# Kernel optimization log

Measured on AMD Instinct MI355X. Metric: run time of the kernel, lower is better.

## Reference

```python
import jax, jax.numpy as jnp
import numpy as np
from jax import lax

COMMITMENT_COST = 0.25

def setup_inputs() -> dict:
    key = jax.random.key(0)
    k1, k2, k3, k4 = jax.random.split(key, 4)
    B, C, H, W, K = 32, 128, 32, 32, 8192
    return {
        "x": jax.random.normal(k1, (B, C, H, W), dtype=jnp.float32),
        "W_lin": jax.random.normal(k2, (C, C), dtype=jnp.float32) * (1.0 / np.sqrt(C)),
        "b_lin": jax.random.normal(k3, (C,), dtype=jnp.float32) * 0.01,
        "emb": jax.random.normal(k4, (K, C), dtype=jnp.float32),
    }

def reference(x, W_lin, b_lin, emb):
    B, C, H, W = x.shape
    K = emb.shape[0]
    # BCHW -> BHWC, then linear projection
    inp = jnp.transpose(x, (0, 2, 3, 1))          # [B,H,W,C]
    inp = inp @ W_lin.T + b_lin                   # nn.Linear
    flat = inp.reshape(-1, C)                     # [N,C], N=B*H*W
    # squared L2 distances to codebook: ||z||^2 + ||e||^2 - 2 z.e
    d = (jnp.sum(flat**2, axis=1, keepdims=True)
         + jnp.sum(emb**2, axis=1)
         - 2.0 * flat @ emb.T)                    # [N,K]
    idx = jnp.argmin(d, axis=1)                   # [N]
    quantized = emb[idx].reshape(inp.shape)       # gather == onehot @ emb
    e_latent = jnp.mean((lax.stop_gradient(quantized) - inp) ** 2)
    q_latent = jnp.mean((quantized - lax.stop_gradient(inp)) ** 2)
    loss = q_latent + COMMITMENT_COST * e_latent
    # straight-through estimator
    quantized_st = inp + lax.stop_gradient(quantized - inp)
    # perplexity from code usage histogram (== mean of one-hot encodings)
    counts = jnp.zeros((K,), dtype=flat.dtype).at[idx].add(1.0)
    avg_probs = counts / flat.shape[0]
    perplexity = jnp.exp(-jnp.sum(avg_probs * jnp.log(avg_probs + 1e-10)))
    out = jnp.transpose(quantized_st, (0, 3, 1, 2))  # back to BCHW
    return (loss, out, perplexity, idx[:, None])
```

## Files before the change

kernel.cpp:

```cpp
#include <hip/hip_runtime.h>
#include <hip/hip_bf16.h>
#include <float.h>

#define NPIX   32768
#define CDIM   128
#define KCB    8192
#define EPS_STOP 0.30f
#define TAUF   0.012f
#define RCAP   8192
#define RCAPA  2048

typedef _Float16 f16x8 __attribute__((ext_vector_type(8)));
typedef float    f32x16 __attribute__((ext_vector_type(16)));

#define WS_EMBFH   0
#define WS_E2      2359296
#define WS_ZWS     2392064
#define WS_CAND    19169280
#define WS_IDX     20217856
#define WS_RLISTA  20348928
#define WS_RLISTB  20381696
#define WS_SCAND   20512768
#define WS_SCANI   21037056
#define WS_COUNTS  21299200
#define WS_LOSS    21331968
#define WS_RCNTA   21331972
#define WS_RCNTB   21331976
#define WS_ZERO_OFF 21299200
#define WS_ZERO_LEN 32780

#define OUT_OFF_OUT  1
#define OUT_OFF_PERP 4194305
#define OUT_OFF_IDX  4194306

__device__ __forceinline__ float min3f(float a, float b, float c) {
    return fminf(fminf(a, b), c);
}

__device__ __forceinline__ void ins6(float f, float v[6]) {
    float a = fmaxf(v[0], f); v[0] = fminf(v[0], f);
    float b = fmaxf(v[1], a); v[1] = fminf(v[1], a);
    a = fmaxf(v[2], b); v[2] = fminf(v[2], b);
    b = fmaxf(v[3], a); v[3] = fminf(v[3], a);
    a = fmaxf(v[4], b); v[4] = fminf(v[4], b);
    v[5] = fminf(v[5], a);
}

__device__ __forceinline__ float packmin(float m, uint32_t id) {
    return __uint_as_float((__float_as_uint(m) & 0xFFFFFE00u) | id);
}

__global__ __launch_bounds__(256) void k_prep2(const float* __restrict__ emb,
                                               _Float16* __restrict__ embFh,
                                               int* __restrict__ zerobuf) {
    const int t = threadIdx.x, w = t >> 6, l = t & 63;
    if (blockIdx.x < 9) {
        int idx0 = blockIdx.x * 1024 + t * 4;
        #pragma unroll
        for (int k = 0; k < 4; ++k)
            if (idx0 + k < 8195) zerobuf[idx0 + k] = 0;
    }
    __shared__ float rs[4][128];
    const int m = blockIdx.x * 4 + w;
    const float2 v = *(const float2*)&emb[(size_t)m * 128 + l * 2];
    rs[w][l * 2] = v.x; rs[w][l * 2 + 1] = v.y;
    float s = v.x * v.x + v.y * v.y;
    #pragma unroll
    for (int o = 32; o; o >>= 1) s += __shfl_down(s, o, 64);
    const float e2v = __shfl(s, 0, 64);

    f16x8 hv;
    #pragma unroll
    for (int j = 0; j < 8; ++j) hv[j] = (_Float16)0.0f;
    if (l < 16) {
        const float* rp = &rs[w][l * 8];
        #pragma unroll
        for (int j = 0; j < 8; ++j) hv[j] = (_Float16)(-2.0f * rp[j]);
    } else if (l == 16) {
        float vv = e2v + 512.0f;
        _Float16 eh = (_Float16)vv;
        hv[0] = eh;
        hv[1] = (_Float16)(vv - (float)eh);
    }
    if (l < 18) {
        const int s_ = l >> 1, h_ = l & 1;
        size_t base = (((size_t)(m >> 5) * 9 + s_) * 64 + (m & 31) + h_ * 32) * 8;
        *(f16x8*)&embFh[base] = hv;
    }
}

__global__ __launch_bounds__(256, 2) void k_main(
    const float* __restrict__ x, const float* __restrict__ Wl, const float* __restrict__ bl,
    const _Float16* __restrict__ embFh,
    float* __restrict__ zws, float4* __restrict__ cand)
{
    __shared__ __align__(16) float As[64 * 132];
    __shared__ __align__(16) float Xs[64 * 66];
    __shared__ float z2p[256];

    const int t  = threadIdx.x;
    const int n0 = blockIdx.x * 64;
    const int b  = n0 >> 10;
    const int hw0 = n0 & 1023;

    {
        const int p = t & 63, ig = t >> 6;
        float accz[32];
        const float4* bl4 = (const float4*)(bl + ig * 32);
        #pragma unroll
        for (int q = 0; q < 8; ++q) {
            float4 v = bl4[q];
            accz[4*q+0] = v.x; accz[4*q+1] = v.y; accz[4*q+2] = v.z; accz[4*q+3] = v.w;
        }
        for (int hf = 0; hf < 2; ++hf) {
            __syncthreads();
            for (int r = 0; r < 16; ++r) {
                int lin = r * 256 + t;
                int cc = lin >> 6, pp = lin & 63;
                Xs[cc * 66 + pp] = x[(size_t)(b * 128 + hf * 64 + cc) * 1024 + hw0 + pp];
            }
            __syncthreads();
            for (int cc4 = 0; cc4 < 16; ++cc4) {
                float xv0 = Xs[(cc4*4+0) * 66 + p];
                float xv1 = Xs[(cc4*4+1) * 66 + p];
                float xv2 = Xs[(cc4*4+2) * 66 + p];
                float xv3 = Xs[(cc4*4+3) * 66 + p];
                #pragma unroll
                for (int ii = 0; ii < 32; ++ii) {
                    const float4 w4 = *(const float4*)&Wl[(size_t)(ig*32+ii) * 128 + hf*64 + cc4*4];
                    float a = accz[ii];
                    a = fmaf(w4.x, xv0, a);
                    a = fmaf(w4.y, xv1, a);
                    a = fmaf(w4.z, xv2, a);
                    a = fmaf(w4.w, xv3, a);
                    accz[ii] = a;
                }
            }
        }
        float ssq = 0.f;
        float4* ao = (float4*)&As[p * 132 + ig * 32];
        float4* zo = (float4*)(zws + (size_t)(n0 + p) * 128 + ig * 32);
        #pragma unroll
        for (int q = 0; q < 8; ++q) {
            float4 v = make_float4(accz[4*q+0], accz[4*q+1], accz[4*q+2], accz[4*q+3]);
            ao[q] = v;
            zo[q] = v;
            ssq = fmaf(v.x, v.x, fmaf(v.y, v.y, fmaf(v.z, v.z, fmaf(v.w, v.w, ssq))));
        }
        z2p[p * 4 + ig] = ssq;
    }
    __syncthreads();

    const int l = t & 63, w = t >> 6;
    const int half = l >> 5, pcol = l & 31;
    f16x8 B0[9], B1[9];
    #pragma unroll
    for (int nt = 0; nt < 2; ++nt) {
        int p = nt * 32 + pcol;
        #pragma unroll
        for (int s = 0; s < 8; ++s) {
            const float* zp = &As[p * 132 + s * 16 + half * 8];
            float4 v0 = *(const float4*)zp;
            float4 v1 = *(const float4*)(zp + 4);
            float vals[8] = {v0.x, v0.y, v0.z, v0.w, v1.x, v1.y, v1.z, v1.w};
            f16x8 hh;
            #pragma unroll
            for (int j2 = 0; j2 < 8; ++j2) hh[j2] = (_Float16)vals[j2];
            if (nt == 0) B0[s] = hh; else B1[s] = hh;
        }
    }
    {
        f16x8 b8;
        #pragma unroll
        for (int j2 = 0; j2 < 8; ++j2) b8[j2] = (_Float16)0.0f;
        if (half == 0) { b8[0] = (_Float16)1.0f; b8[1] = (_Float16)1.0f; }
        B0[8] = b8; B1[8] = b8;
    }

    auto tree16 = [](const f32x16& v) -> float {
        float a = min3f(v[0], v[1], v[2]);
        float bb = min3f(v[3], v[4], v[5]);
        float c = min3f(v[6], v[7], v[8]);
        float d = min3f(v[9], v[10], v[11]);
        float e = min3f(v[12], v[13], v[14]);
        float f = min3f(a, bb, c);
        float g = min3f(d, e, v[15]);
        return fminf(f, g);
    };

    float gv[6] = {3e38f, 3e38f, 3e38f, 3e38f, 3e38f, 3e38f};
    float hv[6] = {3e38f, 3e38f, 3e38f, 3e38f, 3e38f, 3e38f};
    const f16x8* Ahp = (const f16x8*)embFh;
    f16x8 aE[9], aO[9];
    {
        const f16x8* P = Ahp + (size_t)w * 576 + l;
        #pragma unroll
        for (int s = 0; s < 9; ++s) aE[s] = P[s * 64];
    }
    {
        const f16x8* P = Ahp + (size_t)(w + 4) * 576 + l;
        #pragma unroll
        for (int s = 0; s < 9; ++s) aO[s] = P[s * 64];
    }

    f32x16 e0, e1, o0, o1;
    uint32_t idv = (uint32_t)((w << 1) | half);

    e0 = {}; e1 = {};
    #pragma unroll
    for (int s = 0; s < 9; ++s) {
        e0 = __builtin_amdgcn_mfma_f32_32x32x16_f16(aE[s], B0[s], e0, 0, 0, 0);
        e1 = __builtin_amdgcn_mfma_f32_32x32x16_f16(aE[s], B1[s], e1, 0, 0, 0);
    }

    for (int it = 0; it < 31; ++it) {
        const int g = w + it * 8;
        {
            const f16x8* P = Ahp + (size_t)(g + 8) * 576 + l;
            #pragma unroll
            for (int s = 0; s < 9; ++s) aE[s] = P[s * 64];
        }
        o0 = {}; o1 = {};
        #pragma unroll
        for (int s = 0; s < 9; ++s) {
            o0 = __builtin_amdgcn_mfma_f32_32x32x16_f16(aO[s], B0[s], o0, 0, 0, 0);
            o1 = __builtin_amdgcn_mfma_f32_32x32x16_f16(aO[s], B1[s], o1, 0, 0, 0);
        }
        {
            float m0 = tree16(e0), m1 = tree16(e1);
            ins6(packmin(m0, idv), gv);
            ins6(packmin(m1, idv), hv);
        }
        {
            const f16x8* P = Ahp + (size_t)(g + 12) * 576 + l;
            #pragma unroll
            for (int s = 0; s < 9; ++s) aO[s] = P[s * 64];
        }
        e0 = {}; e1 = {};
        #pragma unroll
        for (int s = 0; s < 9; ++s) {
            e0 = __builtin_amdgcn_mfma_f32_32x32x16_f16(aE[s], B0[s], e0, 0, 0, 0);
            e1 = __builtin_amdgcn_mfma_f32_32x32x16_f16(aE[s], B1[s], e1, 0, 0, 0);
        }
        {
            float m0 = tree16(o0), m1 = tree16(o1);
            ins6(packmin(m0, idv + 8u), gv);
            ins6(packmin(m1, idv + 8u), hv);
        }
        idv += 16u;
    }
    o0 = {}; o1 = {};
    #pragma unroll
    for (int s = 0; s < 9; ++s) {
        o0 = __builtin_amdgcn_mfma_f32_32x32x16_f16(aO[s], B0[s], o0, 0, 0, 0);
        o1 = __builtin_amdgcn_mfma_f32_32x32x16_f16(aO[s], B1[s], o1, 0, 0, 0);
    }
    {
        float m0 = tree16(e0), m1 = tree16(e1);
        ins6(packmin(m0, idv), gv);
        ins6(packmin(m1, idv), hv);
    }
    {
        float m0 = tree16(o0), m1 = tree16(o1);
        ins6(packmin(m0, idv + 8u), gv);
        ins6(packmin(m1, idv + 8u), hv);
    }

    __syncthreads();
    float* Ms = Xs;
    const int slot = (w << 1) | half;
    #pragma unroll
    for (int q = 0; q < 6; ++q) {
        Ms[(pcol * 8 + slot) * 6 + q] = gv[q];
        Ms[((32 + pcol) * 8 + slot) * 6 + q] = hv[q];
    }
    __syncthreads();
    if (t < 64) {
        float v6[6] = {3e38f, 3e38f, 3e38f, 3e38f, 3e38f, 3e38f};
        #pragma unroll
        for (int s = 0; s < 48; ++s) ins6(Ms[t * 48 + s], v6);
        float z2 = z2p[t*4+0] + z2p[t*4+1] + z2p[t*4+2] + z2p[t*4+3];
        cand[(size_t)(n0 + t) * 2 + 0] = make_float4(v6[0], v6[1], v6[2], v6[3]);
        cand[(size_t)(n0 + t) * 2 + 1] = make_float4(v6[4], v6[5], z2, 0.f);
    }
}

__global__ __launch_bounds__(256) void k_rec(
    const float* __restrict__ zws, const float* __restrict__ emb,
    const float4* __restrict__ cand, int* __restrict__ idxws,
    float* __restrict__ out_idxf, float* __restrict__ losssum,
    int* __restrict__ rlistA, int* __restrict__ rcntA,
    int* __restrict__ rlistB, int* __restrict__ rcntB)
{
    __shared__ float lred[16];
    const int t = threadIdx.x;
    const int pl = t >> 4, j = t & 15;
    const int n = blockIdx.x * 16 + pl;

    const float4 za = *(const float4*)&zws[(size_t)n * 128 + j * 8];
    const float4 zb = *(const float4*)&zws[(size_t)n * 128 + j * 8 + 4];
    const float4 c0 = cand[(size_t)n * 2 + 0];
    const float4 c1 = cand[(size_t)n * 2 + 1];
    const float pv[6] = {c0.x, c0.y, c0.z, c0.w, c1.x, c1.y};
    const float pbase = c1.z - 512.0f;

    float d1 = 3e38f, d2 = 3e38f; int i1 = 0x7fffffff, i2 = 0x7fffffff;
    bool safe = false;
    float lastgmin = 0.f;
    for (int q = 0; q < 6; ++q) {
        uint32_t bits = __float_as_uint(pv[q]);
        float gmin = __uint_as_float(bits & 0xFFFFFE00u);
        lastgmin = gmin;
        if (gmin >= d1 - pbase + EPS_STOP) { safe = true; break; }
        const int mbase = (int)((bits >> 1) & 255u) * 32 + (int)((bits & 1u) << 2);
        #pragma unroll
        for (int c = 0; c < 16; ++c) {
            int m = mbase + (c & 3) + 8 * (c >> 2);
            const float4 ea = *(const float4*)&emb[(size_t)m * 128 + j * 8];
            const float4 eb = *(const float4*)&emb[(size_t)m * 128 + j * 8 + 4];
            float da0 = za.x - ea.x, da1 = za.y - ea.y, da2 = za.z - ea.z, da3 = za.w - ea.w;
            float db0 = zb.x - eb.x, db1 = zb.y - eb.y, db2 = zb.z - eb.z, db3 = zb.w - eb.w;
            float s0 = da0*da0; s0 = fmaf(da1, da1, s0); s0 = fmaf(da2, da2, s0); s0 = fmaf(da3, da3, s0);
            float s1 = db0*db0; s1 = fmaf(db1, db1, s1); s1 = fmaf(db2, db2, s1); s1 = fmaf(db3, db3, s1);
            float s = s0 + s1;
            s += __shfl_xor(s, 1, 16);
            s += __shfl_xor(s, 2, 16);
            s += __shfl_xor(s, 4, 16);
            s += __shfl_xor(s, 8, 16);
            if (s < d1 || (s == d1 && m < i1)) { d2 = d1; i2 = i1; d1 = s; i1 = m; }
            else if (s < d2) { d2 = s; i2 = m; }
        }
    }
    if (!safe && lastgmin >= d1 - pbase + EPS_STOP) safe = true;

    if (j == 0) {
        idxws[n] = i1;
        out_idxf[n] = (float)i1;
        if (!safe) {
            int s = atomicAdd(rcntA, 1);
            if (s < RCAPA) rlistA[s] = n;
        } else if ((d2 - d1) < TAUF) {
            int s = atomicAdd(rcntB, 1);
            if (s < RCAP) { int4 v4 = make_int4(n, i1, i2, 0); ((int4*)rlistB)[s] = v4; }
        }
        lred[pl] = d1;
    }
    __syncthreads();
    if (t == 0) {
        float ls = 0.f;
        #pragma unroll
        for (int q = 0; q < 16; ++q) ls += lred[q];
        atomicAdd(losssum, ls);
    }
}

__global__ __launch_bounds__(256) void k_scanp(
    const float* __restrict__ zws, const float* __restrict__ emb,
    const int* __restrict__ rcntA, const int* __restrict__ rlistA,
    double* __restrict__ scand, int* __restrict__ scani)
{
    int cnt = *rcntA; if (cnt > RCAPA) cnt = RCAPA;
    const int t = threadIdx.x;
    const int chunk = blockIdx.x & 31;
    const int gi = t >> 4, j = t & 15;
    __shared__ double sd[16];
    __shared__ int si[16];
    for (int e = blockIdx.x >> 5; e < cnt; e += 64) {
        const int n = rlistA[e];
        const float4 za = *(const float4*)&zws[(size_t)n * 128 + j * 8];
        const float4 zb = *(const float4*)&zws[(size_t)n * 128 + j * 8 + 4];
        double best = 1e300; int bi = 0x7fffffff;
        const int kbase = chunk * 256 + gi * 16;
        for (int c = 0; c < 16; ++c) {
            const int m = kbase + c;
            const float4 ea = *(const float4*)&emb[(size_t)m * 128 + j * 8];
            const float4 eb = *(const float4*)&emb[(size_t)m * 128 + j * 8 + 4];
            double sa = 0.0, sb = 0.0, d;
            d = (double)za.x - (double)ea.x; sa += d * d;
            d = (double)za.y - (double)ea.y; sa += d * d;
            d = (double)za.z - (double)ea.z; sa += d * d;
            d = (double)za.w - (double)ea.w; sa += d * d;
            d = (double)zb.x - (double)eb.x; sb += d * d;
            d = (double)zb.y - (double)eb.y; sb += d * d;
            d = (double)zb.z - (double)eb.z; sb += d * d;
            d = (double)zb.w - (double)eb.w; sb += d * d;
            double s = sa + sb;
            s += __shfl_xor(s, 1, 16);
            s += __shfl_xor(s, 2, 16);
            s += __shfl_xor(s, 4, 16);
            s += __shfl_xor(s, 8, 16);
            if (s < best) { best = s; bi = m; }
        }
        __syncthreads();
        if (j == 0) { sd[gi] = best; si[gi] = bi; }
        __syncthreads();
        if (t == 0) {
            double b = sd[0]; int ib = si[0];
            #pragma unroll
            for (int q = 1; q < 16; ++q)
                if (sd[q] < b || (sd[q] == b && si[q] < ib)) { b = sd[q]; ib = si[q]; }
            scand[e * 32 + chunk] = b;
            scani[e * 32 + chunk] = ib;
        }
    }
}

__global__ __launch_bounds__(128) void k_fix(
    const float* __restrict__ x, const float* __restrict__ Wl, const float* __restrict__ bl,
    const float* __restrict__ emb,
    const int* __restrict__ rcntA, const int* __restrict__ rlistA,
    const double* __restrict__ scand, const int* __restrict__ scani,
    const int* __restrict__ rcntB, const int* __restrict__ rlistB,
    int* __restrict__ idxws, float* __restrict__ out_idxf)
{
    const int t = threadIdx.x;
    if (blockIdx.x < 32) {
        if (t < 64) {
            int cnt = *rcntA; if (cnt > RCAPA) cnt = RCAPA;
            for (int e = blockIdx.x; e < cnt; e += 32) {
                double b = 1e300; int ib = 0x7fffffff;
                if (t < 32) { b = scand[e * 32 + t]; ib = scani[e * 32 + t]; }
                #pragma unroll
                for (int o = 16; o; o >>= 1) {
                    double ob = __shfl_down(b, o, 64);
                    int oi = __shfl_down(ib, o, 64);
                    if (ob < b || (ob == b && oi < ib)) { b = ob; ib = oi; }
                }
                if (t == 0) { int n = rlistA[e]; idxws[n] = ib; out_idxf[n] = (float)ib; }
            }
        }
        return;
    }
    __shared__ double xs[128];
    __shared__ double red[128];
    __shared__ double red2[128];
    int cnt = *rcntB; if (cnt > RCAP) cnt = RCAP;
    for (int e = (int)blockIdx.x - 32; e < cnt; e += 256) {
        const int4 v = ((const int4*)rlistB)[e];
        const int n = v.x, c1 = v.y, c2 = v.z;
        const int b = n >> 10, hw = n & 1023;
        __syncthreads();
        xs[t] = (double)x[(size_t)(b * 128 + t) * 1024 + hw];
        __syncthreads();
        double z0 = (double)bl[t], z1 = 0.0, z2 = 0.0, z3 = 0.0;
        const float* wr = &Wl[(size_t)t * 128];
        #pragma unroll 8
        for (int c = 0; c < 128; c += 4) {
            z0 = fma((double)wr[c + 0], xs[c + 0], z0);
            z1 = fma((double)wr[c + 1], xs[c + 1], z1);
            z2 = fma((double)wr[c + 2], xs[c + 2], z2);
            z3 = fma((double)wr[c + 3], xs[c + 3], z3);
        }
        double z = (z0 + z1) + (z2 + z3);
        double da = z - (double)emb[(size_t)c1 * 128 + t];
        double db = z - (double)emb[(size_t)c2 * 128 + t];
        red[t] = da * da; red2[t] = db * db;
        __syncthreads();
        for (int o = 64; o; o >>= 1) {
            if (t < o) { red[t] += red[t + o]; red2[t] += red2[t + o]; }
            __syncthreads();
        }
        if (t == 0) {
            double d1v = red[0], d2v = red2[0];
            int win = (d2v < d1v || (d2v == d1v && c2 < c1)) ? c2 : c1;
            idxws[n] = win;
            out_idxf[n] = (float)win;
        }
        __syncthreads();
    }
}

__global__ __launch_bounds__(256) void k_out(
    const float* __restrict__ emb, const int* __restrict__ idxws,
    float* __restrict__ outp , float* __restrict__ counts)
{
    const int t = threadIdx.x;
    const int b  = blockIdx.x >> 4;
    const int h2 = blockIdx.x & 15;
    const int pix = t & 63;
    const int cq  = t >> 6;
    const int n = b * 1024 + h2 * 64 + pix;
    const int id = idxws[n];
    if (cq == 0) atomicAdd(&counts[id], 1.0f);
    const float4* ep = (const float4*)&emb[(size_t)id * 128 + cq * 32];
    float* ob = outp + (size_t)b * 131072 + (size_t)cq * 32768 + h2 * 64 + pix;
    #pragma unroll
    for (int c4 = 0; c4 < 8; ++c4) {
        float4 v = ep[c4];
        __builtin_nontemporal_store(v.x, &ob[(c4 * 4 + 0) * 1024]);
        __builtin_nontemporal_store(v.y, &ob[(c4 * 4 + 1) * 1024]);
        __builtin_nontemporal_store(v.z, &ob[(c4 * 4 + 2) * 1024]);
        __builtin_nontemporal_store(v.w, &ob[(c4 * 4 + 3) * 1024]);
    }
}

__global__ __launch_bounds__(256) void k_final(
    const float* __restrict__ counts, const float* __restrict__ losssum, float* __restrict__ d_out)
{
    const int t = threadIdx.x;
    float ent = 0.f;
    for (int k = t; k < KCB; k += 256) {
        float p = counts[k] * (1.0f / 32768.0f);
        ent -= p * logf(p + 1e-10f);
    }
    #pragma unroll
    for (int o = 32; o; o >>= 1) ent += __shfl_down(ent, o, 64);
    __shared__ float wred[4];
    if ((t & 63) == 0) wred[t >> 6] = ent;
    __syncthreads();
    if (t == 0) {
        float e = wred[0] + wred[1] + wred[2] + wred[3];
        d_out[0] = 1.25f * (*losssum) * (1.0f / 4194304.0f);
        d_out[OUT_OFF_PERP] = expf(e);
    }
}

extern "C" void kernel_launch(void* const* d_in, const int* in_sizes, int n_in,
                              void* d_out, int out_size, void* d_ws, size_t ws_size,
                              hipStream_t stream) {
    (void)in_sizes; (void)n_in; (void)out_size; (void)ws_size;
    const float* x   = (const float*)d_in[0];
    const float* Wl  = (const float*)d_in[1];
    const float* bl  = (const float*)d_in[2];
    const float* emb = (const float*)d_in[3];
    float* out = (float*)d_out;
    char*  ws  = (char*)d_ws;

    _Float16* embFh = (_Float16*)(ws + WS_EMBFH);
    float* zws     = (float*)(ws + WS_ZWS);
    float4* cand   = (float4*)(ws + WS_CAND);
    int*   idxws   = (int*)  (ws + WS_IDX);
    int*   rlistA  = (int*)  (ws + WS_RLISTA);
    int*   rlistB  = (int*)  (ws + WS_RLISTB);
    double* scand  = (double*)(ws + WS_SCAND);
    int*   scani   = (int*)  (ws + WS_SCANI);
    float* counts  = (float*)(ws + WS_COUNTS);
    float* losssum = (float*)(ws + WS_LOSS);
    int*   rcntA   = (int*)  (ws + WS_RCNTA);
    int*   rcntB   = (int*)  (ws + WS_RCNTB);
    int*   zerobuf = (int*)  (ws + WS_ZERO_OFF);

    k_prep2<<<KCB / 4, 256, 0, stream>>>(emb, embFh, zerobuf);
    k_main<<<NPIX / 64, 256, 0, stream>>>(x, Wl, bl, embFh, zws, cand);
    k_rec<<<NPIX / 16, 256, 0, stream>>>(zws, emb, cand, idxws, out + OUT_OFF_IDX,
                                         losssum, rlistA, rcntA, rlistB, rcntB);
    k_scanp<<<2048, 256, 0, stream>>>(zws, emb, rcntA, rlistA, scand, scani);
    k_fix<<<288, 128, 0, stream>>>(x, Wl, bl, emb, rcntA, rlistA, scand, scani,
                                   rcntB, rlistB, idxws, out + OUT_OFF_IDX);
    k_out<<<512, 256, 0, stream>>>(emb, idxws, out + OUT_OFF_OUT, counts);
    k_final<<<1, 256, 0, stream>>>(counts, losssum, out);
}
```

Baseline: 275.6 us.

## Fuse candidate rescoring kernel into main distance kernel

Moves the exact fp32 rescoring of the top-6 candidate groups from a separate k_rec kernel into the tail of k_main. Candidates and z are read from shared memory (As, candL) rather than written to and re-read from global memory, and one kernel launch goes away. The cost is extra shared memory per block in a kernel tuned for 2 blocks/CU. The serial 4-pass rescoring loop also lengthens each block's tail, which could lower occupancy or overlap.

```diff
diff --git a/kernel.cpp b/kernel.cpp
--- a/kernel.cpp
+++ b/kernel.cpp
@@ -91,12 +91,16 @@
 
 __global__ __launch_bounds__(256, 2) void k_main(
     const float* __restrict__ x, const float* __restrict__ Wl, const float* __restrict__ bl,
-    const _Float16* __restrict__ embFh,
-    float* __restrict__ zws, float4* __restrict__ cand)
+    const _Float16* __restrict__ embFh, const float* __restrict__ emb,
+    float* __restrict__ zws, int* __restrict__ idxws,
+    float* __restrict__ out_idxf, float* __restrict__ losssum,
+    int* __restrict__ rlistA, int* __restrict__ rcntA,
+    int* __restrict__ rlistB, int* __restrict__ rcntB)
 {
     __shared__ __align__(16) float As[64 * 132];
     __shared__ __align__(16) float Xs[64 * 66];
     __shared__ float z2p[256];
+    __shared__ float candL[64 * 8];
 
     const int t  = threadIdx.x;
     const int n0 = blockIdx.x * 64;
@@ -280,77 +284,75 @@
         #pragma unroll
         for (int s = 0; s < 48; ++s) ins6(Ms[t * 48 + s], v6);
         float z2 = z2p[t*4+0] + z2p[t*4+1] + z2p[t*4+2] + z2p[t*4+3];
-        cand[(size_t)(n0 + t) * 2 + 0] = make_float4(v6[0], v6[1], v6[2], v6[3]);
-        cand[(size_t)(n0 + t) * 2 + 1] = make_float4(v6[4], v6[5], z2, 0.f);
-    }
-}
-
-__global__ __launch_bounds__(256) void k_rec(
-    const float* __restrict__ zws, const float* __restrict__ emb,
-    const float4* __restrict__ cand, int* __restrict__ idxws,
-    float* __restrict__ out_idxf, float* __restrict__ losssum,
-    int* __restrict__ rlistA, int* __restrict__ rcntA,
-    int* __restrict__ rlistB, int* __restrict__ rcntB)
-{
-    __shared__ float lred[16];
-    const int t = threadIdx.x;
-    const int pl = t >> 4, j = t & 15;
-    const int n = blockIdx.x * 16 + pl;
-
-    const float4 za = *(const float4*)&zws[(size_t)n * 128 + j * 8];
-    const float4 zb = *(const float4*)&zws[(size_t)n * 128 + j * 8 + 4];
-    const float4 c0 = cand[(size_t)n * 2 + 0];
-    const float4 c1 = cand[(size_t)n * 2 + 1];
-    const float pv[6] = {c0.x, c0.y, c0.z, c0.w, c1.x, c1.y};
-    const float pbase = c1.z - 512.0f;
-
-    float d1 = 3e38f, d2 = 3e38f; int i1 = 0x7fffffff, i2 = 0x7fffffff;
-    bool safe = false;
-    float lastgmin = 0.f;
-    for (int q = 0; q < 6; ++q) {
-        uint32_t bits = __float_as_uint(pv[q]);
-        float gmin = __uint_as_float(bits & 0xFFFFFE00u);
-        lastgmin = gmin;
-        if (gmin >= d1 - pbase + EPS_STOP) { safe = true; break; }
-        const int mbase = (int)((bits >> 1) & 255u) * 32 + (int)((bits & 1u) << 2);
-        #pragma unroll
-        for (int c = 0; c < 16; ++c) {
-            int m = mbase + (c & 3) + 8 * (c >> 2);
-            const float4 ea = *(const float4*)&emb[(size_t)m * 128 + j * 8];
-            const float4 eb = *(const float4*)&emb[(size_t)m * 128 + j * 8 + 4];
-            float da0 = za.x - ea.x, da1 = za.y - ea.y, da2 = za.z - ea.z, da3 = za.w - ea.w;
-            float db0 = zb.x - eb.x, db1 = zb.y - eb.y, db2 = zb.z - eb.z, db3 = zb.w - eb.w;
-            float s0 = da0*da0; s0 = fmaf(da1, da1, s0); s0 = fmaf(da2, da2, s0); s0 = fmaf(da3, da3, s0);
-            float s1 = db0*db0; s1 = fmaf(db1, db1, s1); s1 = fmaf(db2, db2, s1); s1 = fmaf(db3, db3, s1);
-            float s = s0 + s1;
-            s += __shfl_xor(s, 1, 16);
-            s += __shfl_xor(s, 2, 16);
-            s += __shfl_xor(s, 4, 16);
-            s += __shfl_xor(s, 8, 16);
-            if (s < d1 || (s == d1 && m < i1)) { d2 = d1; i2 = i1; d1 = s; i1 = m; }
-            else if (s < d2) { d2 = s; i2 = m; }
-        }
-    }
-    if (!safe && lastgmin >= d1 - pbase + EPS_STOP) safe = true;
-
-    if (j == 0) {
-        idxws[n] = i1;
-        out_idxf[n] = (float)i1;
-        if (!safe) {
-            int s = atomicAdd(rcntA, 1);
-            if (s < RCAPA) rlistA[s] = n;
-        } else if ((d2 - d1) < TAUF) {
-            int s = atomicAdd(rcntB, 1);
-            if (s < RCAP) { int4 v4 = make_int4(n, i1, i2, 0); ((int4*)rlistB)[s] = v4; }
-        }
-        lred[pl] = d1;
+        #pragma unroll
+        for (int q = 0; q < 6; ++q) candL[t * 8 + q] = v6[q];
+        candL[t * 8 + 6] = z2;
     }
     __syncthreads();
-    if (t == 0) {
-        float ls = 0.f;
-        #pragma unroll
-        for (int q = 0; q < 16; ++q) ls += lred[q];
-        atomicAdd(losssum, ls);
+
+    {
+        const int pl = t >> 4, j = t & 15;
+        float lossacc = 0.f;
+        for (int pass = 0; pass < 4; ++pass) {
+            const int px = pass * 16 + pl;
+            const int n = n0 + px;
+            const float4 za = *(const float4*)&As[px * 132 + j * 8];
+            const float4 zb = *(const float4*)&As[px * 132 + j * 8 + 4];
+            const float* cl = &candL[px * 8];
+            const float pv[6] = {cl[0], cl[1], cl[2], cl[3], cl[4], cl[5]};
+            const float pbase = cl[6] - 512.0f;
+
+            float d1 = 3e38f, d2 = 3e38f; int i1 = 0x7fffffff, i2 = 0x7fffffff;
+            bool safe = false;
+            float lastgmin = 0.f;
+            for (int q = 0; q < 6; ++q) {
+                uint32_t bits = __float_as_uint(pv[q]);
+                float gmin = __uint_as_float(bits & 0xFFFFFE00u);
+                lastgmin = gmin;
+                if (gmin >= d1 - pbase + EPS_STOP) { safe = true; break; }
+                const int mbase = (int)((bits >> 1) & 255u) * 32 + (int)((bits & 1u) << 2);
+                #pragma unroll
+                for (int c = 0; c < 16; ++c) {
+                    int m = mbase + (c & 3) + 8 * (c >> 2);
+                    const float4 ea = *(const float4*)&emb[(size_t)m * 128 + j * 8];
+                    const float4 eb = *(const float4*)&emb[(size_t)m * 128 + j * 8 + 4];
+                    float da0 = za.x - ea.x, da1 = za.y - ea.y, da2 = za.z - ea.z, da3 = za.w - ea.w;
+                    float db0 = zb.x - eb.x, db1 = zb.y - eb.y, db2 = zb.z - eb.z, db3 = zb.w - eb.w;
+                    float s0 = da0*da0; s0 = fmaf(da1, da1, s0); s0 = fmaf(da2, da2, s0); s0 = fmaf(da3, da3, s0);
+                    float s1 = db0*db0; s1 = fmaf(db1, db1, s1); s1 = fmaf(db2, db2, s1); s1 = fmaf(db3, db3, s1);
+                    float s = s0 + s1;
+                    s += __shfl_xor(s, 1, 16);
+                    s += __shfl_xor(s, 2, 16);
+                    s += __shfl_xor(s, 4, 16);
+                    s += __shfl_xor(s, 8, 16);
+                    if (s < d1 || (s == d1 && m < i1)) { d2 = d1; i2 = i1; d1 = s; i1 = m; }
+                    else if (s < d2) { d2 = s; i2 = m; }
+                }
+            }
+            if (!safe && lastgmin >= d1 - pbase + EPS_STOP) safe = true;
+
+            if (j == 0) {
+                idxws[n] = i1;
+                out_idxf[n] = (float)i1;
+                if (!safe) {
+                    int s = atomicAdd(rcntA, 1);
+                    if (s < RCAPA) rlistA[s] = n;
+                } else if ((d2 - d1) < TAUF) {
+                    int s = atomicAdd(rcntB, 1);
+                    if (s < RCAP) { int4 v4 = make_int4(n, i1, i2, 0); ((int4*)rlistB)[s] = v4; }
+                }
+                lossacc += d1;
+            }
+        }
+        __syncthreads();
+        if (j == 0) z2p[pl] = lossacc;
+        __syncthreads();
+        if (t == 0) {
+            float ls = 0.f;
+            #pragma unroll
+            for (int q = 0; q < 16; ++q) ls += z2p[q];
+            atomicAdd(losssum, ls);
+        }
     }
 }
 
@@ -528,7 +530,6 @@
 
     _Float16* embFh = (_Float16*)(ws + WS_EMBFH);
     float* zws     = (float*)(ws + WS_ZWS);
-    float4* cand   = (float4*)(ws + WS_CAND);
     int*   idxws   = (int*)  (ws + WS_IDX);
     int*   rlistA  = (int*)  (ws + WS_RLISTA);
     int*   rlistB  = (int*)  (ws + WS_RLISTB);
@@ -541,9 +542,9 @@
     int*   zerobuf = (int*)  (ws + WS_ZERO_OFF);
 
     k_prep2<<<KCB / 4, 256, 0, stream>>>(emb, embFh, zerobuf);
-    k_main<<<NPIX / 64, 256, 0, stream>>>(x, Wl, bl, embFh, zws, cand);
-    k_rec<<<NPIX / 16, 256, 0, stream>>>(zws, emb, cand, idxws, out + OUT_OFF_IDX,
-                                         losssum, rlistA, rcntA, rlistB, rcntB);
+    k_main<<<NPIX / 64, 256, 0, stream>>>(x, Wl, bl, embFh, emb, zws, idxws,
+                                          out + OUT_OFF_IDX, losssum,
+                                          rlistA, rcntA, rlistB, rcntB);
     k_scanp<<<2048, 256, 0, stream>>>(zws, emb, rcntA, rlistA, scand, scani);
     k_fix<<<288, 128, 0, stream>>>(x, Wl, bl, emb, rcntA, rlistA, scand, scani,
                                    rcntB, rlistB, idxws, out + OUT_OFF_IDX);
```

Measured after the change: 283.9 us. 3.0% more time.

## Split k_main work across 512 threads with one pixel tile per wave

Applied to the files above, without the earlier changes.

Doubles the block size of k_main to 512 threads. Each wave now handles one 32-pixel column tile against a quarter of the codebook, instead of two pixel tiles against an eighth, so each wave keeps a single B fragment set and one top-6 list. The projection is split so each thread computes 16 output channels rather than 32. The goal is to cut register pressure and raise occupancy to hide MFMA and load latency. The cost is that each wave now loads codebook A fragments for half as many MFMAs, doubling codebook global/L2 traffic per block.

```diff
diff --git a/kernel.cpp b/kernel.cpp
--- a/kernel.cpp
+++ b/kernel.cpp
@@ -89,14 +89,14 @@
     }
 }
 
-__global__ __launch_bounds__(256, 2) void k_main(
+__global__ __launch_bounds__(512, 4) void k_main(
     const float* __restrict__ x, const float* __restrict__ Wl, const float* __restrict__ bl,
     const _Float16* __restrict__ embFh,
     float* __restrict__ zws, float4* __restrict__ cand)
 {
     __shared__ __align__(16) float As[64 * 132];
     __shared__ __align__(16) float Xs[64 * 66];
-    __shared__ float z2p[256];
+    __shared__ float z2p[64 * 8];
 
     const int t  = threadIdx.x;
     const int n0 = blockIdx.x * 64;
@@ -105,17 +105,17 @@
 
     {
         const int p = t & 63, ig = t >> 6;
-        float accz[32];
-        const float4* bl4 = (const float4*)(bl + ig * 32);
-        #pragma unroll
-        for (int q = 0; q < 8; ++q) {
+        float accz[16];
+        const float4* bl4 = (const float4*)(bl + ig * 16);
+        #pragma unroll
+        for (int q = 0; q < 4; ++q) {
             float4 v = bl4[q];
             accz[4*q+0] = v.x; accz[4*q+1] = v.y; accz[4*q+2] = v.z; accz[4*q+3] = v.w;
         }
         for (int hf = 0; hf < 2; ++hf) {
             __syncthreads();
-            for (int r = 0; r < 16; ++r) {
-                int lin = r * 256 + t;
+            for (int r = 0; r < 8; ++r) {
+                int lin = r * 512 + t;
                 int cc = lin >> 6, pp = lin & 63;
                 Xs[cc * 66 + pp] = x[(size_t)(b * 128 + hf * 64 + cc) * 1024 + hw0 + pp];
             }
@@ -126,8 +126,8 @@
                 float xv2 = Xs[(cc4*4+2) * 66 + p];
                 float xv3 = Xs[(cc4*4+3) * 66 + p];
                 #pragma unroll
-                for (int ii = 0; ii < 32; ++ii) {
-                    const float4 w4 = *(const float4*)&Wl[(size_t)(ig*32+ii) * 128 + hf*64 + cc4*4];
+                for (int ii = 0; ii < 16; ++ii) {
+                    const float4 w4 = *(const float4*)&Wl[(size_t)(ig*16+ii) * 128 + hf*64 + cc4*4];
                     float a = accz[ii];
                     a = fmaf(w4.x, xv0, a);
                     a = fmaf(w4.y, xv1, a);
@@ -138,43 +138,40 @@
             }
         }
         float ssq = 0.f;
-        float4* ao = (float4*)&As[p * 132 + ig * 32];
-        float4* zo = (float4*)(zws + (size_t)(n0 + p) * 128 + ig * 32);
-        #pragma unroll
-        for (int q = 0; q < 8; ++q) {
+        float4* ao = (float4*)&As[p * 132 + ig * 16];
+        float4* zo = (float4*)(zws + (size_t)(n0 + p) * 128 + ig * 16);
+        #pragma unroll
+        for (int q = 0; q < 4; ++q) {
             float4 v = make_float4(accz[4*q+0], accz[4*q+1], accz[4*q+2], accz[4*q+3]);
             ao[q] = v;
             zo[q] = v;
             ssq = fmaf(v.x, v.x, fmaf(v.y, v.y, fmaf(v.z, v.z, fmaf(v.w, v.w, ssq))));
         }
-        z2p[p * 4 + ig] = ssq;
+        z2p[p * 8 + ig] = ssq;
     }
     __syncthreads();
 
     const int l = t & 63, w = t >> 6;
     const int half = l >> 5, pcol = l & 31;
-    f16x8 B0[9], B1[9];
+    const int px = ((w >> 2) << 5) + pcol;
+    f16x8 B[9];
     #pragma unroll
-    for (int nt = 0; nt < 2; ++nt) {
-        int p = nt * 32 + pcol;
-        #pragma unroll
-        for (int s = 0; s < 8; ++s) {
-            const float* zp = &As[p * 132 + s * 16 + half * 8];
-            float4 v0 = *(const float4*)zp;
-            float4 v1 = *(const float4*)(zp + 4);
-            float vals[8] = {v0.x, v0.y, v0.z, v0.w, v1.x, v1.y, v1.z, v1.w};
-            f16x8 hh;
-            #pragma unroll
-            for (int j2 = 0; j2 < 8; ++j2) hh[j2] = (_Float16)vals[j2];
-            if (nt == 0) B0[s] = hh; else B1[s] = hh;
-        }
+    for (int s = 0; s < 8; ++s) {
+        const float* zp = &As[px * 132 + s * 16 + half * 8];
+        float4 v0 = *(const float4*)zp;
+        float4 v1 = *(const float4*)(zp + 4);
+        float vals[8] = {v0.x, v0.y, v0.z, v0.w, v1.x, v1.y, v1.z, v1.w};
+        f16x8 hh;
+        #pragma unroll
+        for (int j2 = 0; j2 < 8; ++j2) hh[j2] = (_Float16)vals[j2];
+        B[s] = hh;
     }
     {
         f16x8 b8;
         #pragma unroll
         for (int j2 = 0; j2 < 8; ++j2) b8[j2] = (_Float16)0.0f;
         if (half == 0) { b8[0] = (_Float16)1.0f; b8[1] = (_Float16)1.0f; }
-        B0[8] = b8; B1[8] = b8;
+        B[8] = b8;
     }
 
     auto tree16 = [](const f32x16& v) -> float {
@@ -189,97 +186,61 @@
     };
 
     float gv[6] = {3e38f, 3e38f, 3e38f, 3e38f, 3e38f, 3e38f};
-    float hv[6] = {3e38f, 3e38f, 3e38f, 3e38f, 3e38f, 3e38f};
     const f16x8* Ahp = (const f16x8*)embFh;
-    f16x8 aE[9], aO[9];
-    {
-        const f16x8* P = Ahp + (size_t)w * 576 + l;
-        #pragma unroll
-        for (int s = 0; s < 9; ++s) aE[s] = P[s * 64];
-    }
-    {
-        const f16x8* P = Ahp + (size_t)(w + 4) * 576 + l;
-        #pragma unroll
-        for (int s = 0; s < 9; ++s) aO[s] = P[s * 64];
-    }
-
-    f32x16 e0, e1, o0, o1;
-    uint32_t idv = (uint32_t)((w << 1) | half);
-
-    e0 = {}; e1 = {};
-    #pragma unroll
-    for (int s = 0; s < 9; ++s) {
-        e0 = __builtin_amdgcn_mfma_f32_32x32x16_f16(aE[s], B0[s], e0, 0, 0, 0);
-        e1 = __builtin_amdgcn_mfma_f32_32x32x16_f16(aE[s], B1[s], e1, 0, 0, 0);
-    }
-
-    for (int it = 0; it < 31; ++it) {
-        const int g = w + it * 8;
-        {
-            const f16x8* P = Ahp + (size_t)(g + 8) * 576 + l;
-            #pragma unroll
-            for (int s = 0; s < 9; ++s) aE[s] = P[s * 64];
-        }
-        o0 = {}; o1 = {};
-        #pragma unroll
-        for (int s = 0; s < 9; ++s) {
-            o0 = __builtin_amdgcn_mfma_f32_32x32x16_f16(aO[s], B0[s], o0, 0, 0, 0);
-            o1 = __builtin_amdgcn_mfma_f32_32x32x16_f16(aO[s], B1[s], o1, 0, 0, 0);
-        }
-        {
-            float m0 = tree16(e0), m1 = tree16(e1);
-            ins6(packmin(m0, idv), gv);
-            ins6(packmin(m1, idv), hv);
-        }
-        {
-            const f16x8* P = Ahp + (size_t)(g + 12) * 576 + l;
-            #pragma unroll
-            for (int s = 0; s < 9; ++s) aO[s] = P[s * 64];
-        }
-        e0 = {}; e1 = {};
-        #pragma unroll
-        for (int s = 0; s < 9; ++s) {
-            e0 = __builtin_amdgcn_mfma_f32_32x32x16_f16(aE[s], B0[s], e0, 0, 0, 0);
-            e1 = __builtin_amdgcn_mfma_f32_32x32x16_f16(aE[s], B1[s], e1, 0, 0, 0);
-        }
-        {
-            float m0 = tree16(o0), m1 = tree16(o1);
-            ins6(packmin(m0, idv + 8u), gv);
-            ins6(packmin(m1, idv + 8u), hv);
-        }
-        idv += 16u;
-    }
-    o0 = {}; o1 = {};
-    #pragma unroll
-    for (int s = 0; s < 9; ++s) {
-        o0 = __builtin_amdgcn_mfma_f32_32x32x16_f16(aO[s], B0[s], o0, 0, 0, 0);
-        o1 = __builtin_amdgcn_mfma_f32_32x32x16_f16(aO[s], B1[s], o1, 0, 0, 0);
-    }
-    {
-        float m0 = tree16(e0), m1 = tree16(e1);
-        ins6(packmin(m0, idv), gv);
-        ins6(packmin(m1, idv), hv);
-    }
-    {
-        float m0 = tree16(o0), m1 = tree16(o1);
-        ins6(packmin(m0, idv + 8u), gv);
-        ins6(packmin(m1, idv + 8u), hv);
-    }
+    const int gbase = w & 3;
+    f16x8 a[9];
+    f32x16 P, Q;
+
+    #define LOADA(i_) { \
+        const f16x8* Pp = Ahp + (size_t)(gbase + 4 * (i_)) * 576 + l; \
+        _Pragma("unroll") \
+        for (int s_ = 0; s_ < 9; ++s_) a[s_] = Pp[s_ * 64]; \
+    }
+    #define BURST(C_) { \
+        C_ = (f32x16){}; \
+        _Pragma("unroll") \
+        for (int s_ = 0; s_ < 9; ++s_) \
+            C_ = __builtin_amdgcn_mfma_f32_32x32x16_f16(a[s_], B[s_], C_, 0, 0, 0); \
+    }
+    #define TAIL(C_, i_) { \
+        float m0_ = tree16(C_); \
+        uint32_t id_ = (uint32_t)(((gbase + 4 * (i_)) << 1) | half); \
+        ins6(packmin(m0_, id_), gv); \
+    }
+
+    LOADA(0);
+    BURST(P);
+    LOADA(1);
+    #pragma unroll 1
+    for (int i = 0; i < 31; ++i) {
+        BURST(Q);
+        LOADA(2 * i + 2);
+        TAIL(P, 2 * i);
+        BURST(P);
+        LOADA(2 * i + 3);
+        TAIL(Q, 2 * i + 1);
+    }
+    BURST(Q);
+    TAIL(P, 62);
+    TAIL(Q, 63);
+
+    #undef LOADA
+    #undef BURST
+    #undef TAIL
 
     __syncthreads();
     float* Ms = Xs;
-    const int slot = (w << 1) | half;
+    const int slot = ((w & 3) << 1) | half;
     #pragma unroll
-    for (int q = 0; q < 6; ++q) {
-        Ms[(pcol * 8 + slot) * 6 + q] = gv[q];
-        Ms[((32 + pcol) * 8 + slot) * 6 + q] = hv[q];
-    }
+    for (int q = 0; q < 6; ++q) Ms[(px * 8 + slot) * 6 + q] = gv[q];
     __syncthreads();
     if (t < 64) {
         float v6[6] = {3e38f, 3e38f, 3e38f, 3e38f, 3e38f, 3e38f};
         #pragma unroll
         for (int s = 0; s < 48; ++s) ins6(Ms[t * 48 + s], v6);
-        float z2 = z2p[t*4+0] + z2p[t*4+1] + z2p[t*4+2] + z2p[t*4+3];
+        float z2 = 0.f;
+        #pragma unroll
+        for (int q = 0; q < 8; ++q) z2 += z2p[t * 8 + q];
         cand[(size_t)(n0 + t) * 2 + 0] = make_float4(v6[0], v6[1], v6[2], v6[3]);
         cand[(size_t)(n0 + t) * 2 + 1] = make_float4(v6[4], v6[5], z2, 0.f);
     }
@@ -541,7 +502,7 @@
     int*   zerobuf = (int*)  (ws + WS_ZERO_OFF);
 
     k_prep2<<<KCB / 4, 256, 0, stream>>>(emb, embFh, zerobuf);
-    k_main<<<NPIX / 64, 256, 0, stream>>>(x, Wl, bl, embFh, zws, cand);
+    k_main<<<NPIX / 64, 512, 0, stream>>>(x, Wl, bl, embFh, zws, cand);
     k_rec<<<NPIX / 16, 256, 0, stream>>>(zws, emb, cand, idxws, out + OUT_OFF_IDX,
                                          losssum, rlistA, rcntA, rlistB, rcntB);
     k_scanp<<<2048, 256, 0, stream>>>(zws, emb, rcntA, rlistA, scand, scani);
```

New measurement: 317.8 us. +15.3%, slower.
